# Performance work log

Measured on AMD Instinct MI355X. Metric: run time of the kernel, lower is better.

Reference implementation:

```python
import jax, jax.numpy as jnp
import numpy as np

S = 32          # input grid resolution
N = 2048        # active input voxels
C = 256         # in channels
CO = 128        # out channels
S2 = 2 * S      # upsampled resolution
M = 8 * N       # candidate child voxels
EPS = 1e-6


def setup_inputs() -> dict:
    key = jax.random.key(0)
    ks = jax.random.split(key, 8)
    # unique voxel coordinates (sparse occupancy)
    lin = jax.random.permutation(ks[0], S ** 3)[:N]
    coords = jnp.stack([lin // (S * S), (lin // S) % S, lin % S], axis=-1).astype(jnp.int32)
    sc = 0.05
    return {
        "feats": jax.random.normal(ks[1], (N, C), jnp.float32),
        "norm1_w": 1.0 + 0.1 * jax.random.normal(ks[2], (C,), jnp.float32),
        "norm1_b": 0.1 * jax.random.normal(ks[3], (C,), jnp.float32),
        "subdiv_w": sc * jax.random.normal(ks[4], (C, 8), jnp.float32),
        "subdiv_b": jnp.zeros((8,), jnp.float32),
        "conv1_w": sc * jax.random.normal(ks[5], (27, C, CO), jnp.float32),
        "conv1_b": jnp.zeros((CO,), jnp.float32),
        "conv2_w": sc * jax.random.normal(ks[6], (27, CO, CO), jnp.float32),
        "conv2_b": jnp.zeros((CO,), jnp.float32),
        "skip_w": sc * jax.random.normal(ks[7], (C, CO), jnp.float32),
        "skip_b": jnp.zeros((CO,), jnp.float32),
        "coords": coords,
    }


def _layernorm(x, w=None, b=None):
    # LayerNorm32: fp32 math, eps=1e-6
    m = jnp.mean(x, axis=-1, keepdims=True)
    v = jnp.var(x, axis=-1, keepdims=True)
    y = (x - m) * jax.lax.rsqrt(v + EPS)
    if w is not None:
        y = y * w + b
    return y


def _sparse_conv(feats, nidx, w, b):
    # submanifold 3x3x3 sparse conv: gather 27 neighbors, contract.
    # nidx: [M,27] with sentinel M pointing at a zero row.
    pad = jnp.concatenate([feats, jnp.zeros((1, feats.shape[1]), feats.dtype)], axis=0)
    g = pad[nidx]                                   # [M, 27, Cin]
    return jnp.einsum('nkc,kcd->nd', g, w) + b


def _forward(feats, norm1_w, norm1_b, subdiv_w, subdiv_b, conv1_w, conv1_b,
             conv2_w, conv2_b, skip_w, skip_b, coords):
    # subdiv prediction (SparseLinear C -> 8)
    subdiv = feats @ subdiv_w + subdiv_b            # [N, 8]
    # norm1 + silu
    h = jax.nn.silu(_layernorm(feats, norm1_w, norm1_b))
    # sparse upsample x2 with octree subdivision mask
    mask = (subdiv > 0).reshape(-1)                 # [M]
    j = jnp.arange(8, dtype=jnp.int32)
    offs8 = jnp.stack([(j >> 2) & 1, (j >> 1) & 1, j & 1], axis=-1)  # [8,3]
    cc = (coords[:, None, :] * 2 + offs8[None]).reshape(-1, 3)        # [M,3]
    h_c = jnp.where(mask[:, None], jnp.repeat(h, 8, axis=0), 0.0)     # [M,C]
    x_c = jnp.where(mask[:, None], jnp.repeat(feats, 8, axis=0), 0.0)
    # neighbor lookup grid (padded by 1; default M -> zero feature row)
    grid = jnp.full((S2 + 2, S2 + 2, S2 + 2), M, jnp.int32)
    grid = grid.at[cc[:, 0] + 1, cc[:, 1] + 1, cc[:, 2] + 1].set(
        jnp.arange(M, dtype=jnp.int32))
    d = jnp.arange(-1, 2, dtype=jnp.int32)
    offs27 = jnp.stack(jnp.meshgrid(d, d, d, indexing='ij'), axis=-1).reshape(27, 3)
    nc = cc[:, None, :] + 1 + offs27[None]          # [M,27,3]
    nidx = grid[nc[..., 0], nc[..., 1], nc[..., 2]] # [M,27]
    # conv1 -> norm2 (no affine) -> silu -> conv2
    h1 = jax.nn.silu(_layernorm(_sparse_conv(h_c, nidx, conv1_w, conv1_b)))
    h2 = _sparse_conv(h1, nidx, conv2_w, conv2_b)
    # residual with linear skip; mask out non-subdivided children
    out = (h2 + x_c @ skip_w + skip_b) * mask[:, None].astype(h2.dtype)
    return out, subdiv


def reference(feats, norm1_w, norm1_b, subdiv_w, subdiv_b, conv1_w, conv1_b,
              conv2_w, conv2_b, skip_w, skip_b, coords):
    return _forward(feats, norm1_w, norm1_b, subdiv_w, subdiv_b, conv1_w,
                    conv1_b, conv2_w, conv2_b, skip_w, skip_b, coords)
```

## Files before the change

kernel.cpp:

```cpp
#include <hip/hip_runtime.h>
#include <cstdint>
#include <cstddef>

constexpr int N  = 2048;
constexpr int C  = 256;
constexpr int CO = 128;
constexpr int M  = 16384;
constexpr int G  = 66;
constexpr int KP = 7;
constexpr int KCHUNK = 4;
constexpr float EPS = 1e-6f;

using bf8 = __attribute__((ext_vector_type(8))) short;
using f4  = __attribute__((ext_vector_type(4))) float;

static __device__ __forceinline__ unsigned short f2bf(float f) {
  unsigned u = __float_as_uint(f);
  u += 0x7fffu + ((u >> 16) & 1u);
  return (unsigned short)(u >> 16);
}
static __device__ __forceinline__ float bf2f(unsigned short s) {
  return __uint_as_float((unsigned)s << 16);
}

__global__ void k_prep(int* __restrict__ grid, unsigned short* __restrict__ h,
                       unsigned short* __restrict__ h1,
                       const float* __restrict__ c1w, unsigned short* __restrict__ w1t,
                       const float* __restrict__ c2w, unsigned short* __restrict__ w2t) {
  int i = blockIdx.x * 256 + threadIdx.x;
  if (i < G * G * G) grid[i] = M;
  if (i < C)  h[(size_t)N * C + i] = 0;
  if (i < CO) h1[(size_t)M * CO + i] = 0;
  if (i < 27 * C * CO) {
    int c = i % C;
    int rest = i / C;
    int o = rest % CO;
    int k = rest / CO;
    w1t[i] = f2bf(c1w[((size_t)(k * C + c)) * CO + o]);
  }
  if (i < 27 * CO * CO) {
    int c = i % CO;
    int rest = i / CO;
    int o = rest % CO;
    int k = rest / CO;
    w2t[i] = f2bf(c2w[((size_t)(k * CO + c)) * CO + o]);
  }
}

__global__ __launch_bounds__(256) void k_rownorm(
    const float* __restrict__ feats, const float* __restrict__ n1w,
    const float* __restrict__ n1b, const float* __restrict__ sdw,
    const float* __restrict__ sdb, float* __restrict__ out_subdiv,
    unsigned short* __restrict__ h, int* __restrict__ pidx,
    float* __restrict__ maskf, const int* __restrict__ coords,
    int* __restrict__ grid) {
  int n = blockIdx.x, t = threadIdx.x;
  float x = feats[(size_t)n * C + t];
  float4 w0 = *(const float4*)(sdw + t * 8);
  float4 w1 = *(const float4*)(sdw + t * 8 + 4);
  float v[10] = {x * w0.x, x * w0.y, x * w0.z, x * w0.w,
                 x * w1.x, x * w1.y, x * w1.z, x * w1.w, x, x * x};
#pragma unroll
  for (int mk = 1; mk < 64; mk <<= 1) {
#pragma unroll
    for (int j = 0; j < 10; ++j) v[j] += __shfl_xor(v[j], mk, 64);
  }
  __shared__ float red[4][10];
  int wave = t >> 6, lane = t & 63;
  if (lane == 0) {
#pragma unroll
    for (int j = 0; j < 10; ++j) red[wave][j] = v[j];
  }
  __syncthreads();
  float sums[10];
#pragma unroll
  for (int j = 0; j < 10; ++j)
    sums[j] = red[0][j] + red[1][j] + red[2][j] + red[3][j];
  float mean = sums[8] / (float)C;
  float var  = sums[9] / (float)C - mean * mean;
  float rstd = rsqrtf(var + EPS);
  if (t < 8) {
    float sd = sums[t] + sdb[t];
    out_subdiv[(size_t)n * 8 + t] = sd;
    bool mk = sd > 0.f;
    pidx[n * 8 + t]  = mk ? n : N;
    maskf[n * 8 + t] = mk ? 1.f : 0.f;
    int xx = coords[n * 3 + 0] * 2 + ((t >> 2) & 1) + 1;
    int yy = coords[n * 3 + 1] * 2 + ((t >> 1) & 1) + 1;
    int zz = coords[n * 3 + 2] * 2 + (t & 1) + 1;
    grid[(xx * G + yy) * G + zz] = n * 8 + t;
  }
  float y  = (x - mean) * rstd * n1w[t] + n1b[t];
  float sl = y / (1.f + __expf(-y));
  h[(size_t)n * C + t] = f2bf(sl);
}

__global__ void k_nidx(const int* __restrict__ coords, const int* __restrict__ grid,
                       const int* __restrict__ pidx, int* __restrict__ nidxt,
                       int* __restrict__ g1t) {
  int idx = blockIdx.x * 256 + threadIdx.x;
  if (idx >= M * 27) return;
  int m = idx & (M - 1);
  int k = idx >> 14;
  int p = m >> 3, j = m & 7;
  int dx = k / 9 - 1;
  int dy = (k / 3) % 3 - 1;
  int dz = k % 3 - 1;
  int x = coords[p * 3 + 0] * 2 + ((j >> 2) & 1) + 1 + dx;
  int y = coords[p * 3 + 1] * 2 + ((j >> 1) & 1) + 1 + dy;
  int z = coords[p * 3 + 2] * 2 + (j & 1) + 1 + dz;
  int gv = grid[(x * G + y) * G + z];
  nidxt[idx] = gv;
  g1t[idx] = (gv == M) ? N : pidx[gv];
}

__global__ __launch_bounds__(256) void k_skip(const float* __restrict__ feats,
                                              const float* __restrict__ skw,
                                              const float* __restrict__ skb,
                                              float* __restrict__ s) {
  __shared__ float tile[32][36];
  int t = threadIdx.x;
  int rb = (blockIdx.x >> 1) * 32;
  int ob = (blockIdx.x & 1) * 64;
  int o = ob + (t & 63);
  int rg = (t >> 6) * 8;
  float acc[8] = {0, 0, 0, 0, 0, 0, 0, 0};
  for (int cb = 0; cb < C; cb += 32) {
    __syncthreads();
    int row = t >> 3, cc = (t & 7) * 4;
    *(float4*)&tile[row][cc] =
        *(const float4*)(feats + (size_t)(rb + row) * C + cb + cc);
    __syncthreads();
    for (int c = 0; c < 32; ++c) {
      float wv = skw[(size_t)(cb + c) * CO + o];
#pragma unroll
      for (int r = 0; r < 8; ++r) acc[r] += tile[rg + r][c] * wv;
    }
  }
  float bv = skb[o];
#pragma unroll
  for (int r = 0; r < 8; ++r) s[(size_t)(rb + rg + r) * CO + o] = acc[r] + bv;
}

template <int CIN, int NCB>
__global__ __launch_bounds__(256, 3) void k_conv(
    const unsigned short* __restrict__ src, const int* __restrict__ gt,
    const unsigned short* __restrict__ wt, unsigned short* __restrict__ part) {
  __shared__ unsigned short sA[2][128 * 32];
  __shared__ unsigned short sB[2][128 * 32];
  const int t = threadIdx.x;
  const int w = t >> 6, lane = t & 63;
  const int quad = lane >> 4, ln = lane & 15;
  const int m0 = blockIdx.x * 128;
  const int kpart = blockIdx.y;
  const int k0 = kpart * KCHUNK;
  const int nk = min(KCHUNK, 27 - k0);
  const int nstage = nk * NCB;
  const int rh = (w >> 1) * 64, ch = (w & 1) * 64;

  const int row2 = t >> 1;
  const int c0 = (t & 1) * 2;
  const int x3 = (row2 >> 1) & 3;
  const int wsl0 = row2 * 32 + ((c0) ^ x3) * 8;
  const int wsl1 = row2 * 32 + ((c0 + 1) ^ x3) * 8;

  int ga[KCHUNK];
#pragma unroll
  for (int kk = 0; kk < KCHUNK; ++kk)
    ga[kk] = (kk < nk) ? gt[(size_t)(k0 + kk) * M + m0 + row2] : 0;

  bf8 ra0, ra1, rb0, rb1;
  auto loadreg = [&](int s) {
    const int kk = s / NCB;
    const int cb = s - kk * NCB;
    const unsigned short* pa = src + (size_t)ga[kk] * CIN + cb * 32 + c0 * 8;
    const unsigned short* pb =
        wt + ((size_t)(k0 + kk) * CO + row2) * CIN + cb * 32 + c0 * 8;
    ra0 = *(const bf8*)(pa);
    ra1 = *(const bf8*)(pa + 8);
    rb0 = *(const bf8*)(pb);
    rb1 = *(const bf8*)(pb + 8);
  };
  auto writelds = [&](int buf) {
    *(bf8*)(sA[buf] + wsl0) = ra0;
    *(bf8*)(sA[buf] + wsl1) = ra1;
    *(bf8*)(sB[buf] + wsl0) = rb0;
    *(bf8*)(sB[buf] + wsl1) = rb1;
  };

  f4 acc[16];
  f4 zero = {0.f, 0.f, 0.f, 0.f};
#pragma unroll
  for (int i = 0; i < 16; ++i) acc[i] = zero;

  const int slot = (quad ^ ((ln >> 1) & 3)) * 8;

  loadreg(0);
  writelds(0);
  for (int s = 0; s < nstage; ++s) {
    const bool have = (s + 1 < nstage);
    if (have) loadreg(s + 1);
    __syncthreads();
    const unsigned short* pa = sA[s & 1];
    const unsigned short* pb = sB[s & 1];
    bf8 av[4], bv[4];
#pragma unroll
    for (int ti = 0; ti < 4; ++ti)
      av[ti] = *(const bf8*)(pa + (rh + ti * 16 + ln) * 32 + slot);
#pragma unroll
    for (int tj = 0; tj < 4; ++tj)
      bv[tj] = *(const bf8*)(pb + (ch + tj * 16 + ln) * 32 + slot);
#pragma unroll
    for (int ti = 0; ti < 4; ++ti)
#pragma unroll
      for (int tj = 0; tj < 4; ++tj)
        acc[ti * 4 + tj] = __builtin_amdgcn_mfma_f32_16x16x32_bf16(
            av[ti], bv[tj], acc[ti * 4 + tj], 0, 0, 0);
    if (have) writelds((s + 1) & 1);
  }

  unsigned short* pp = part + ((size_t)kpart * M + m0) * CO;
#pragma unroll
  for (int ti = 0; ti < 4; ++ti) {
    int mrow = rh + ti * 16 + quad * 4;
#pragma unroll
    for (int tj = 0; tj < 4; ++tj) {
      int co = ch + tj * 16 + ln;
#pragma unroll
      for (int rr = 0; rr < 4; ++rr)
        pp[(size_t)(mrow + rr) * CO + co] = f2bf(acc[ti * 4 + tj][rr]);
    }
  }
}

__global__ __launch_bounds__(256) void k_r1(const unsigned short* __restrict__ p,
                                            const float* __restrict__ bias,
                                            unsigned short* __restrict__ h1) {
  int wave = threadIdx.x >> 6, lane = threadIdx.x & 63;
  int m = blockIdx.x * 4 + wave;
  float v0 = bias[lane], v1 = bias[lane + 64];
#pragma unroll
  for (int q = 0; q < KP; ++q) {
    const unsigned short* pq = p + ((size_t)q * M + m) * CO;
    v0 += bf2f(pq[lane]);
    v1 += bf2f(pq[lane + 64]);
  }
  float sum = v0 + v1, sq = v0 * v0 + v1 * v1;
#pragma unroll
  for (int mk = 1; mk < 64; mk <<= 1) {
    sum += __shfl_xor(sum, mk, 64);
    sq  += __shfl_xor(sq, mk, 64);
  }
  float mean = sum / (float)CO;
  float var  = sq / (float)CO - mean * mean;
  float rstd = rsqrtf(var + EPS);
  float y0 = (v0 - mean) * rstd;
  float y1 = (v1 - mean) * rstd;
  float s0 = y0 / (1.f + __expf(-y0));
  float s1 = y1 / (1.f + __expf(-y1));
  h1[(size_t)m * CO + lane]      = f2bf(s0);
  h1[(size_t)m * CO + lane + 64] = f2bf(s1);
}

__global__ __launch_bounds__(256) void k_r2(const unsigned short* __restrict__ p,
                                            const float* __restrict__ bias,
                                            const float* __restrict__ sres,
                                            const float* __restrict__ maskf,
                                            float* __restrict__ out) {
  int i = blockIdx.x * 256 + threadIdx.x;
  int m = i >> 5;
  int o4 = (i & 31) * 4;
  float4 acc = *(const float4*)(bias + o4);
#pragma unroll
  for (int q = 0; q < KP; ++q) {
    ushort4 a = *(const ushort4*)(p + ((size_t)q * M + m) * CO + o4);
    acc.x += bf2f(a.x); acc.y += bf2f(a.y);
    acc.z += bf2f(a.z); acc.w += bf2f(a.w);
  }
  float4 s = *(const float4*)(sres + (size_t)(m >> 3) * CO + o4);
  float mk = maskf[m];
  float4 r;
  r.x = (acc.x + s.x) * mk;
  r.y = (acc.y + s.y) * mk;
  r.z = (acc.z + s.z) * mk;
  r.w = (acc.w + s.w) * mk;
  *(float4*)(out + (size_t)m * CO + o4) = r;
}

extern "C" void kernel_launch(void* const* d_in, const int* in_sizes, int n_in,
                              void* d_out, int out_size, void* d_ws, size_t ws_size,
                              hipStream_t stream) {
  const float* feats = (const float*)d_in[0];
  const float* n1w   = (const float*)d_in[1];
  const float* n1b   = (const float*)d_in[2];
  const float* sdw   = (const float*)d_in[3];
  const float* sdb   = (const float*)d_in[4];
  const float* c1w   = (const float*)d_in[5];
  const float* c1b   = (const float*)d_in[6];
  const float* c2w   = (const float*)d_in[7];
  const float* c2b   = (const float*)d_in[8];
  const float* skw   = (const float*)d_in[9];
  const float* skb   = (const float*)d_in[10];
  const int* coords  = (const int*)d_in[11];
  float* out = (float*)d_out;

  char* ws = (char*)d_ws;
  size_t off = 0;
  auto alloc = [&](size_t bytes) -> char* {
    char* p = ws + off;
    off += (bytes + 255) & ~(size_t)255;
    return p;
  };
  unsigned short* h    = (unsigned short*)alloc((size_t)(N + 1) * C * 2);
  unsigned short* h1   = (unsigned short*)alloc((size_t)(M + 1) * CO * 2);
  int*   grid  = (int*)alloc((size_t)G * G * G * 4);
  int*   nidxt = (int*)alloc((size_t)27 * M * 4);
  int*   g1t   = (int*)alloc((size_t)27 * M * 4);
  int*   pidx  = (int*)alloc((size_t)M * 4);
  float* maskf = (float*)alloc((size_t)M * 4);
  float* sres  = (float*)alloc((size_t)N * CO * 4);
  unsigned short* w1t = (unsigned short*)alloc((size_t)27 * CO * C * 2);
  unsigned short* w2t = (unsigned short*)alloc((size_t)27 * CO * CO * 2);
  unsigned short* pc  = (unsigned short*)alloc((size_t)KP * M * CO * 2);

  k_prep<<<(27 * C * CO + 255) / 256, 256, 0, stream>>>(grid, h, h1, c1w, w1t,
                                                        c2w, w2t);
  k_rownorm<<<N, 256, 0, stream>>>(feats, n1w, n1b, sdw, sdb,
                                   out + (size_t)M * CO, h, pidx, maskf,
                                   coords, grid);
  k_nidx<<<(M * 27 + 255) / 256, 256, 0, stream>>>(coords, grid, pidx, nidxt, g1t);
  k_skip<<<128, 256, 0, stream>>>(feats, skw, skb, sres);

  k_conv<C, 8><<<dim3(M / 128, KP), 256, 0, stream>>>(h, g1t, w1t, pc);
  k_r1<<<M / 4, 256, 0, stream>>>(pc, c1b, h1);

  k_conv<CO, 4><<<dim3(M / 128, KP), 256, 0, stream>>>(h1, nidxt, w2t, pc);
  k_r2<<<M * CO / 4 / 256, 256, 0, stream>>>(pc, c2b, sres, maskf, out);
}
```

Before: 190.9 us.

## Compute conv1 on parent voxels once per offset, then gather-sum per child

Because children of the same parent share features, conv1 is restructured as a dense GEMM of the N parent rows against all 27 weight slices, written to an fp32 table U of shape [N, 27*CO]. A new kernel then gathers and sums the 27 relevant rows per child and fuses bias, layernorm and SiLU, replacing the partial-sum buffer and k_r1. This cuts conv1 MFMA work by roughly 8x in exchange for a large fp32 intermediate (about 28 MB) and scattered reads. Conv2 now uses 4 K-partitions of 7 offsets instead of 7 of 4, which reduces partial-sum traffic but exposes less parallelism.

```diff
diff --git a/kernel.cpp b/kernel.cpp
--- a/kernel.cpp
+++ b/kernel.cpp
@@ -7,8 +7,9 @@
 constexpr int CO = 128;
 constexpr int M  = 16384;
 constexpr int G  = 66;
-constexpr int KP = 7;
-constexpr int KCHUNK = 4;
+constexpr int KP2 = 4;
+constexpr int KCHUNK2 = 7;
+constexpr int UW = 27 * CO;
 constexpr float EPS = 1e-6f;
 
 using bf8 = __attribute__((ext_vector_type(8))) short;
@@ -143,6 +144,119 @@
 }
 
 template <int CIN, int NCB>
+__global__ __launch_bounds__(256, 3) void k_dgemm(
+    const unsigned short* __restrict__ src, const unsigned short* __restrict__ wt,
+    float* __restrict__ U) {
+  __shared__ unsigned short sA[2][128 * 32];
+  __shared__ unsigned short sB[2][128 * 32];
+  const int t = threadIdx.x;
+  const int w = t >> 6, lane = t & 63;
+  const int quad = lane >> 4, ln = lane & 15;
+  const int m0 = blockIdx.x * 128;
+  const int k = blockIdx.y;
+  const int rh = (w >> 1) * 64, ch = (w & 1) * 64;
+
+  const int row2 = t >> 1;
+  const int c0 = (t & 1) * 2;
+  const int x3 = (row2 >> 1) & 3;
+  const int wsl0 = row2 * 32 + ((c0) ^ x3) * 8;
+  const int wsl1 = row2 * 32 + ((c0 + 1) ^ x3) * 8;
+
+  const unsigned short* pa_base = src + (size_t)(m0 + row2) * CIN + c0 * 8;
+  const unsigned short* pb_base =
+      wt + ((size_t)k * CO + row2) * CIN + c0 * 8;
+
+  bf8 ra0, ra1, rb0, rb1;
+  auto loadreg = [&](int s) {
+    const unsigned short* pa = pa_base + s * 32;
+    const unsigned short* pb = pb_base + s * 32;
+    ra0 = *(const bf8*)(pa);
+    ra1 = *(const bf8*)(pa + 8);
+    rb0 = *(const bf8*)(pb);
+    rb1 = *(const bf8*)(pb + 8);
+  };
+  auto writelds = [&](int buf) {
+    *(bf8*)(sA[buf] + wsl0) = ra0;
+    *(bf8*)(sA[buf] + wsl1) = ra1;
+    *(bf8*)(sB[buf] + wsl0) = rb0;
+    *(bf8*)(sB[buf] + wsl1) = rb1;
+  };
+
+  f4 acc[16];
+  f4 zero = {0.f, 0.f, 0.f, 0.f};
+#pragma unroll
+  for (int i = 0; i < 16; ++i) acc[i] = zero;
+
+  const int slot = (quad ^ ((ln >> 1) & 3)) * 8;
+
+  loadreg(0);
+  writelds(0);
+  for (int s = 0; s < NCB; ++s) {
+    const bool have = (s + 1 < NCB);
+    if (have) loadreg(s + 1);
+    __syncthreads();
+    const unsigned short* pa = sA[s & 1];
+    const unsigned short* pb = sB[s & 1];
+    bf8 av[4], bv[4];
+#pragma unroll
+    for (int ti = 0; ti < 4; ++ti)
+      av[ti] = *(const bf8*)(pa + (rh + ti * 16 + ln) * 32 + slot);
+#pragma unroll
+    for (int tj = 0; tj < 4; ++tj)
+      bv[tj] = *(const bf8*)(pb + (ch + tj * 16 + ln) * 32 + slot);
+#pragma unroll
+    for (int ti = 0; ti < 4; ++ti)
+#pragma unroll
+      for (int tj = 0; tj < 4; ++tj)
+        acc[ti * 4 + tj] = __builtin_amdgcn_mfma_f32_16x16x32_bf16(
+            av[ti], bv[tj], acc[ti * 4 + tj], 0, 0, 0);
+    if (have) writelds((s + 1) & 1);
+  }
+
+#pragma unroll
+  for (int ti = 0; ti < 4; ++ti) {
+    int mrow = rh + ti * 16 + quad * 4;
+#pragma unroll
+    for (int tj = 0; tj < 4; ++tj) {
+      int co = ch + tj * 16 + ln;
+#pragma unroll
+      for (int rr = 0; rr < 4; ++rr)
+        U[(size_t)(m0 + mrow + rr) * UW + k * CO + co] = acc[ti * 4 + tj][rr];
+    }
+  }
+}
+
+__global__ __launch_bounds__(256) void k_g1sum(
+    const float* __restrict__ U, const int* __restrict__ g1t,
+    const float* __restrict__ b1, unsigned short* __restrict__ h1) {
+  int wave = threadIdx.x >> 6, lane = threadIdx.x & 63;
+  int m = blockIdx.x * 4 + wave;
+  float a0 = b1[2 * lane], a1 = b1[2 * lane + 1];
+#pragma unroll
+  for (int k = 0; k < 27; ++k) {
+    int g = g1t[k * M + m];
+    if (g < N) {
+      float2 v = *(const float2*)(U + (size_t)g * UW + k * CO + 2 * lane);
+      a0 += v.x; a1 += v.y;
+    }
+  }
+  float sum = a0 + a1, sq = a0 * a0 + a1 * a1;
+#pragma unroll
+  for (int mk = 1; mk < 64; mk <<= 1) {
+    sum += __shfl_xor(sum, mk, 64);
+    sq  += __shfl_xor(sq, mk, 64);
+  }
+  float mean = sum / (float)CO;
+  float var  = sq / (float)CO - mean * mean;
+  float rstd = rsqrtf(var + EPS);
+  float y0 = (a0 - mean) * rstd;
+  float y1 = (a1 - mean) * rstd;
+  float s0 = y0 / (1.f + __expf(-y0));
+  float s1 = y1 / (1.f + __expf(-y1));
+  *(ushort2*)(h1 + (size_t)m * CO + 2 * lane) = ushort2{f2bf(s0), f2bf(s1)};
+}
+
+template <int CIN, int NCB, int KCH>
 __global__ __launch_bounds__(256, 3) void k_conv(
     const unsigned short* __restrict__ src, const int* __restrict__ gt,
     const unsigned short* __restrict__ wt, unsigned short* __restrict__ part) {
@@ -153,8 +267,8 @@
   const int quad = lane >> 4, ln = lane & 15;
   const int m0 = blockIdx.x * 128;
   const int kpart = blockIdx.y;
-  const int k0 = kpart * KCHUNK;
-  const int nk = min(KCHUNK, 27 - k0);
+  const int k0 = kpart * KCH;
+  const int nk = min(KCH, 27 - k0);
   const int nstage = nk * NCB;
   const int rh = (w >> 1) * 64, ch = (w & 1) * 64;
 
@@ -164,9 +278,9 @@
   const int wsl0 = row2 * 32 + ((c0) ^ x3) * 8;
   const int wsl1 = row2 * 32 + ((c0 + 1) ^ x3) * 8;
 
-  int ga[KCHUNK];
-#pragma unroll
-  for (int kk = 0; kk < KCHUNK; ++kk)
+  int ga[KCH];
+#pragma unroll
+  for (int kk = 0; kk < KCH; ++kk)
     ga[kk] = (kk < nk) ? gt[(size_t)(k0 + kk) * M + m0 + row2] : 0;
 
   bf8 ra0, ra1, rb0, rb1;
@@ -233,35 +347,6 @@
   }
 }
 
-__global__ __launch_bounds__(256) void k_r1(const unsigned short* __restrict__ p,
-                                            const float* __restrict__ bias,
-                                            unsigned short* __restrict__ h1) {
-  int wave = threadIdx.x >> 6, lane = threadIdx.x & 63;
-  int m = blockIdx.x * 4 + wave;
-  float v0 = bias[lane], v1 = bias[lane + 64];
-#pragma unroll
-  for (int q = 0; q < KP; ++q) {
-    const unsigned short* pq = p + ((size_t)q * M + m) * CO;
-    v0 += bf2f(pq[lane]);
-    v1 += bf2f(pq[lane + 64]);
-  }
-  float sum = v0 + v1, sq = v0 * v0 + v1 * v1;
-#pragma unroll
-  for (int mk = 1; mk < 64; mk <<= 1) {
-    sum += __shfl_xor(sum, mk, 64);
-    sq  += __shfl_xor(sq, mk, 64);
-  }
-  float mean = sum / (float)CO;
-  float var  = sq / (float)CO - mean * mean;
-  float rstd = rsqrtf(var + EPS);
-  float y0 = (v0 - mean) * rstd;
-  float y1 = (v1 - mean) * rstd;
-  float s0 = y0 / (1.f + __expf(-y0));
-  float s1 = y1 / (1.f + __expf(-y1));
-  h1[(size_t)m * CO + lane]      = f2bf(s0);
-  h1[(size_t)m * CO + lane + 64] = f2bf(s1);
-}
-
 __global__ __launch_bounds__(256) void k_r2(const unsigned short* __restrict__ p,
                                             const float* __restrict__ bias,
                                             const float* __restrict__ sres,
@@ -272,7 +357,7 @@
   int o4 = (i & 31) * 4;
   float4 acc = *(const float4*)(bias + o4);
 #pragma unroll
-  for (int q = 0; q < KP; ++q) {
+  for (int q = 0; q < KP2; ++q) {
     ushort4 a = *(const ushort4*)(p + ((size_t)q * M + m) * CO + o4);
     acc.x += bf2f(a.x); acc.y += bf2f(a.y);
     acc.z += bf2f(a.z); acc.w += bf2f(a.w);
@@ -321,7 +406,8 @@
   float* sres  = (float*)alloc((size_t)N * CO * 4);
   unsigned short* w1t = (unsigned short*)alloc((size_t)27 * CO * C * 2);
   unsigned short* w2t = (unsigned short*)alloc((size_t)27 * CO * CO * 2);
-  unsigned short* pc  = (unsigned short*)alloc((size_t)KP * M * CO * 2);
+  float* U = (float*)alloc((size_t)N * UW * 4);
+  unsigned short* pc  = (unsigned short*)alloc((size_t)KP2 * M * CO * 2);
 
   k_prep<<<(27 * C * CO + 255) / 256, 256, 0, stream>>>(grid, h, h1, c1w, w1t,
                                                         c2w, w2t);
@@ -331,9 +417,9 @@
   k_nidx<<<(M * 27 + 255) / 256, 256, 0, stream>>>(coords, grid, pidx, nidxt, g1t);
   k_skip<<<128, 256, 0, stream>>>(feats, skw, skb, sres);
 
-  k_conv<C, 8><<<dim3(M / 128, KP), 256, 0, stream>>>(h, g1t, w1t, pc);
-  k_r1<<<M / 4, 256, 0, stream>>>(pc, c1b, h1);
-
-  k_conv<CO, 4><<<dim3(M / 128, KP), 256, 0, stream>>>(h1, nidxt, w2t, pc);
+  k_dgemm<C, 8><<<dim3(N / 128, 27), 256, 0, stream>>>(h, w1t, U);
+  k_g1sum<<<M / 4, 256, 0, stream>>>(U, g1t, c1b, h1);
+
+  k_conv<CO, 4, KCHUNK2><<<dim3(M / 128, KP2), 256, 0, stream>>>(h1, nidxt, w2t, pc);
   k_r2<<<M * CO / 4 / 256, 256, 0, stream>>>(pc, c2b, sres, maskf, out);
 }
```

New measurement: 179.9 us. 5.7% less time.
